# Kernel optimization log

Hardware: AMD Instinct MI355X
Metric: run time of the kernel (lower is better)

Reference implementation:

```python
import jax, jax.numpy as jnp
import numpy as np

B, N, D = 16, 1024, 320
L, H, K = 256, 256, 5
PAIR_IN = 2 * D + 6 + L  # 902


def setup_inputs() -> dict:
    key = jax.random.key(0)
    ks = jax.random.split(key, 8)
    return {
        "object_features": jax.random.normal(ks[0], (B, N, D), jnp.float32),
        "language_embedding": jax.random.normal(ks[1], (B, L), jnp.float32),
        "centers": jax.random.normal(ks[2], (B, N, 3), jnp.float32),
        "sizes": jax.random.uniform(ks[3], (B, N, 3), jnp.float32),
        "object_mask": jnp.ones((B, N), dtype=bool),
        "W1": jax.random.normal(ks[4], (PAIR_IN, H), jnp.float32) * 0.02,
        "b1": jnp.zeros((H,), jnp.float32),
        "W2": jax.random.normal(ks[5], (H, 1), jnp.float32) * 0.02,
        "b2": jnp.zeros((1,), jnp.float32),
    }


def _gather_neighbors(x, idx):
    # x: [B, N, C], idx: [B, N, k] -> [B, N, k, C]
    b, n, c = x.shape
    k = idx.shape[-1]
    flat = jnp.take_along_axis(x, idx.reshape(b, n * k)[..., None], axis=1)
    return flat.reshape(b, n, k, c)


def reference(object_features, language_embedding, centers, sizes, object_mask,
              W1, b1, W2, b2):
    b, n, d = object_features.shape
    k = min(K, n - 1)
    # pairwise squared distances [B, N, N]
    diff = centers[:, :, None, :] - centers[:, None, :, :]
    dist = jnp.sum(diff * diff, axis=-1)
    pair_mask = object_mask[:, :, None] & object_mask[:, None, :]
    dist = jnp.where(pair_mask, dist, jnp.inf)
    dist = jnp.where(jnp.eye(n, dtype=bool)[None], jnp.inf, dist)
    # k nearest neighbors (smallest distance)
    _, neighbor_indices = jax.lax.top_k(-dist, k)  # [B, N, k]

    neighbor_feats = _gather_neighbors(object_features, neighbor_indices)  # [B,N,k,D]
    neighbor_centers = _gather_neighbors(centers, neighbor_indices)        # [B,N,k,3]
    neighbor_sizes = _gather_neighbors(sizes, neighbor_indices)            # [B,N,k,3]

    rel_pos = (centers[:, :, None, :] - neighbor_centers) / 5.0
    rel_size = (sizes[:, :, None, :] - neighbor_sizes) / 2.0

    feat_i = jnp.broadcast_to(object_features[:, :, None, :], (b, n, k, d))
    lang = jnp.broadcast_to(language_embedding[:, None, None, :], (b, n, k, language_embedding.shape[-1]))
    pair_input = jnp.concatenate([feat_i, neighbor_feats, rel_pos, rel_size, lang], axis=-1)

    # relation MLP (dropout is identity in eval)
    h = jax.nn.relu(jnp.einsum('bnkp,ph->bnkh', pair_input, W1) + b1)
    scores = (jnp.einsum('bnkh,ho->bnko', h, W2) + b2)[..., 0]  # [B,N,k]
    weights = jax.nn.softmax(scores, axis=2)

    context = jnp.einsum('bnk,bnkd->bnd', weights, neighbor_feats)
    enhanced = object_features + context  # use_residual=True
    return enhanced, weights, neighbor_indices
```

## Files before the change

### kernel.cpp

```cpp
#include <hip/hip_runtime.h>
#include <math.h>

#define NB 16
#define NN 1024
#define ND 320
#define NL 256
#define NH 256
#define NK 5
#define KE 352

typedef short bf16x8 __attribute__((ext_vector_type(8)));
typedef float f32x4 __attribute__((ext_vector_type(4)));

__device__ inline ushort f2bf(float f) {
    unsigned u = __float_as_uint(f);
    u += 0x7fff + ((u >> 16) & 1);
    return (ushort)(u >> 16);
}
__device__ inline float bf2f(ushort u) {
    return __uint_as_float(((unsigned)u) << 16);
}

__global__ __launch_bounds__(256) void mini_prep_kernel(const float* __restrict__ W1,
                                                        ushort* __restrict__ W1T,
                                                        const float* __restrict__ lang,
                                                        const float* __restrict__ b1,
                                                        float* __restrict__ LP) {
    __shared__ float red[4][64];
    int bid = blockIdx.x;
    if (bid < 512) {
        int n = bid;
        int rowbase = (n < 256) ? 0 : 320;
        int col = n & 255;
        float sign = (n < 256) ? 1.f : -1.f;
        for (int k = threadIdx.x; k < KE; k += 256) {
            float v;
            if (k < 320) v = W1[(rowbase + k) * NH + col];
            else if (k < 326) v = sign * W1[(640 + (k - 320)) * NH + col];
            else v = 0.f;
            W1T[n * KE + k] = f2bf(v);
        }
        return;
    }
    int id = bid - 512;
    int b = id >> 2, hq = id & 3;
    int w = threadIdx.x >> 6, lane = threadIdx.x & 63;
    int h = hq * 64 + lane;
    const float* lb = lang + b * NL;
    float acc = 0.f;
    int l0 = w * 64;
#pragma unroll 8
    for (int l = 0; l < 64; ++l)
        acc = fmaf(lb[l0 + l], W1[(646 + l0 + l) * NH + h], acc);
    red[w][lane] = acc;
    __syncthreads();
    if (w == 0)
        LP[b * NH + h] = b1[h] + red[0][lane] + red[1][lane]
                       + red[2][lane] + red[3][lane];
}

#define LDP 40
__global__ __launch_bounds__(256) void mfma_gemm_kernel(const float* __restrict__ A32,
                                                        const float* __restrict__ C3,
                                                        const float* __restrict__ S3,
                                                        const ushort* __restrict__ BT,
                                                        ushort* __restrict__ P) {
    __shared__ ushort Als[128 * LDP];
    __shared__ ushort Bls[128 * LDP];
    int t = threadIdx.x;
    int lane = t & 63;
    int w = t >> 6;
    int wrow = (w >> 1) * 64, wcol = (w & 1) * 64;
    int m0 = blockIdx.x * 128, n0 = blockIdx.y * 128;
    int lr = lane & 15;
    int lg = lane >> 4;

    f32x4 zero = {0.f, 0.f, 0.f, 0.f};
    f32x4 acc[4][4];
#pragma unroll
    for (int i = 0; i < 4; ++i)
#pragma unroll
        for (int j = 0; j < 4; ++j) acc[i][j] = zero;

    for (int ks = 0; ks < 11; ++ks) {
        int k0 = ks * 32;
#pragma unroll
        for (int it = 0; it < 2; ++it) {
            int s = it * 256 + t;
            int r = s >> 2, q = s & 3;
            int4 pk;
            if (ks < 10) {
                const float* src = &A32[(m0 + r) * ND + k0 + q * 8];
                float4 v0 = *(const float4*)src;
                float4 v1 = *(const float4*)(src + 4);
                pk.x = (int)f2bf(v0.x) | ((int)f2bf(v0.y) << 16);
                pk.y = (int)f2bf(v0.z) | ((int)f2bf(v0.w) << 16);
                pk.z = (int)f2bf(v1.x) | ((int)f2bf(v1.y) << 16);
                pk.w = (int)f2bf(v1.z) | ((int)f2bf(v1.w) << 16);
            } else {
                pk.x = 0; pk.y = 0; pk.z = 0; pk.w = 0;
                if (q == 0) {
                    int m = m0 + r;
                    float c0 = C3[m * 3 + 0] * 0.2f;
                    float c1 = C3[m * 3 + 1] * 0.2f;
                    float c2 = C3[m * 3 + 2] * 0.2f;
                    float s0 = S3[m * 3 + 0] * 0.5f;
                    float s1 = S3[m * 3 + 1] * 0.5f;
                    float s2 = S3[m * 3 + 2] * 0.5f;
                    pk.x = (int)f2bf(c0) | ((int)f2bf(c1) << 16);
                    pk.y = (int)f2bf(c2) | ((int)f2bf(s0) << 16);
                    pk.z = (int)f2bf(s1) | ((int)f2bf(s2) << 16);
                }
            }
            *(int4*)&Als[r * LDP + q * 8] = pk;
            *(int4*)&Bls[r * LDP + q * 8] =
                *(const int4*)&BT[(n0 + r) * KE + k0 + q * 8];
        }
        __syncthreads();
        bf16x8 af[4], bfr[4];
#pragma unroll
        for (int i = 0; i < 4; ++i) {
            af[i]  = *(bf16x8*)&Als[(wrow + i * 16 + lr) * LDP + lg * 8];
            bfr[i] = *(bf16x8*)&Bls[(wcol + i * 16 + lr) * LDP + lg * 8];
        }
#pragma unroll
        for (int i = 0; i < 4; ++i)
#pragma unroll
            for (int j = 0; j < 4; ++j)
                acc[i][j] = __builtin_amdgcn_mfma_f32_16x16x32_bf16(af[i], bfr[j],
                                                                    acc[i][j], 0, 0, 0);
        __syncthreads();
    }

#pragma unroll
    for (int i = 0; i < 4; ++i) {
#pragma unroll
        for (int j = 0; j < 4; ++j) {
            int col = n0 + wcol + j * 16 + lr;
#pragma unroll
            for (int e = 0; e < 4; ++e) {
                int row = m0 + wrow + i * 16 + lg * 4 + e;
                P[row * 512 + col] = f2bf(acc[i][j][e]);
            }
        }
    }
}

#define INS(d, j, D0, D1, D2, D3, D4, I0, I1, I2, I3, I4)                      \
    {                                                                          \
        bool c0 = d < D0, c1 = d < D1, c2 = d < D2, c3 = d < D3, c4 = d < D4;  \
        D4 = c4 ? (c3 ? D3 : d) : D4;  I4 = c4 ? (c3 ? I3 : j) : I4;           \
        D3 = c3 ? (c2 ? D2 : d) : D3;  I3 = c3 ? (c2 ? I2 : j) : I3;           \
        D2 = c2 ? (c1 ? D1 : d) : D2;  I2 = c2 ? (c1 ? I1 : j) : I2;           \
        D1 = c1 ? (c0 ? D0 : d) : D1;  I1 = c1 ? (c0 ? I0 : j) : I1;           \
        D0 = c0 ? d : D0;              I0 = c0 ? j : I0;                       \
    }

__global__ __launch_bounds__(256) void knn_score_kernel(const float* __restrict__ feats,
                                                        const float* __restrict__ centers,
                                                        const ushort* __restrict__ P,
                                                        const float* __restrict__ LP,
                                                        const float* __restrict__ W2,
                                                        const float* __restrict__ b2,
                                                        float* __restrict__ enhanced,
                                                        float* __restrict__ weights,
                                                        float* __restrict__ idx_f) {
    __shared__ float cxs[NN], cys[NN], czs[NN];
    int wave = threadIdx.x >> 6;
    int lane = threadIdx.x & 63;
    int sbid = (blockIdx.x & 7) * 256 + (blockIdx.x >> 3);
    int wv = sbid * 4 + wave;
    int rowA = wv * 2, rowB = rowA | 1;
    int b = rowA >> 10;
    int iA = rowA & (NN - 1), iB = iA + 1;

    const float* cbase = centers + b * (NN * 3);
    for (int j = threadIdx.x; j < NN; j += 256) {
        int o = j * 3;
        cxs[j] = cbase[o]; cys[j] = cbase[o + 1]; czs[j] = cbase[o + 2];
    }
    __syncthreads();

    float pxA = cxs[iA], pyA = cys[iA], pzA = czs[iA];
    float pxB = cxs[iB], pyB = cys[iB], pzB = czs[iB];

    float dA0 = INFINITY, dA1 = INFINITY, dA2 = INFINITY, dA3 = INFINITY, dA4 = INFINITY;
    float dB0 = INFINITY, dB1 = INFINITY, dB2 = INFINITY, dB3 = INFINITY, dB4 = INFINITY;
    int iA0 = -1, iA1 = -1, iA2 = -1, iA3 = -1, iA4 = -1;
    int iB0 = -1, iB1 = -1, iB2 = -1, iB3 = -1, iB4 = -1;

#pragma unroll
    for (int tt = 0; tt < 16; ++tt) {
        int j = tt * 64 + lane;
        float cx = cxs[j], cy = cys[j], cz = czs[j];
        float dxA = pxA - cx, dyA = pyA - cy, dzA = pzA - cz;
        float dA = fmaf(dzA, dzA, fmaf(dyA, dyA, dxA * dxA));
        dA = (j == iA) ? INFINITY : dA;
        float dxB = pxB - cx, dyB = pyB - cy, dzB = pzB - cz;
        float dB = fmaf(dzB, dzB, fmaf(dyB, dyB, dxB * dxB));
        dB = (j == iB) ? INFINITY : dB;
        INS(dA, j, dA0, dA1, dA2, dA3, dA4, iA0, iA1, iA2, iA3, iA4);
        INS(dB, j, dB0, dB1, dB2, dB3, dB4, iB0, iB1, iB2, iB3, iB4);
    }

    int jnA[NK], jnB[NK];
#pragma unroll
    for (int k = 0; k < NK; ++k) {
        float mdA = dA0, mdB = dB0;
        int mjA = iA0, mjB = iB0;
#pragma unroll
        for (int off = 32; off > 0; off >>= 1) {
            float odA = __shfl_xor(mdA, off);
            int ojA = __shfl_xor(mjA, off);
            float odB = __shfl_xor(mdB, off);
            int ojB = __shfl_xor(mjB, off);
            bool tA = (odA < mdA) || ((odA == mdA) && ((unsigned)ojA < (unsigned)mjA));
            bool tB = (odB < mdB) || ((odB == mdB) && ((unsigned)ojB < (unsigned)mjB));
            mdA = tA ? odA : mdA;  mjA = tA ? ojA : mjA;
            mdB = tB ? odB : mdB;  mjB = tB ? ojB : mjB;
        }
        jnA[k] = mjA;
        jnB[k] = mjB;
        bool cA = (iA0 == mjA);
        dA0 = cA ? dA1 : dA0;  iA0 = cA ? iA1 : iA0;
        dA1 = cA ? dA2 : dA1;  iA1 = cA ? iA2 : iA1;
        dA2 = cA ? dA3 : dA2;  iA2 = cA ? iA3 : iA2;
        dA3 = cA ? dA4 : dA3;  iA3 = cA ? iA4 : iA3;
        dA4 = cA ? INFINITY : dA4;
        bool cB = (iB0 == mjB);
        dB0 = cB ? dB1 : dB0;  iB0 = cB ? iB1 : iB0;
        dB1 = cB ? dB2 : dB1;  iB1 = cB ? iB2 : iB1;
        dB2 = cB ? dB3 : dB2;  iB2 = cB ? iB3 : iB2;
        dB3 = cB ? dB4 : dB3;  iB3 = cB ? iB4 : iB3;
        dB4 = cB ? INFINITY : dB4;
    }

    if (lane == 0) {
#pragma unroll
        for (int k = 0; k < NK; ++k) {
            idx_f[rowA * NK + k] = (float)jnA[k];
            idx_f[rowB * NK + k] = (float)jnB[k];
        }
    }

    float4 lpv = ((const float4*)LP)[b * 64 + lane];
    ushort4 pfA = *(const ushort4*)&P[rowA * 512 + (lane << 2)];
    ushort4 pfB = *(const ushort4*)&P[rowB * 512 + (lane << 2)];
    float4 baseA = make_float4(bf2f(pfA.x) + lpv.x, bf2f(pfA.y) + lpv.y,
                               bf2f(pfA.z) + lpv.z, bf2f(pfA.w) + lpv.w);
    float4 baseB = make_float4(bf2f(pfB.x) + lpv.x, bf2f(pfB.y) + lpv.y,
                               bf2f(pfB.z) + lpv.z, bf2f(pfB.w) + lpv.w);
    float4 w2v = ((const float4*)W2)[lane];
    float b2v = b2[0];

    int pbase = (b << 10) * 512 + 256 + (lane << 2);
    float pA[NK], pB[NK];
#pragma unroll
    for (int k = 0; k < NK; ++k) {
        ushort4 pnA = *(const ushort4*)&P[pbase + jnA[k] * 512];
        ushort4 pnB = *(const ushort4*)&P[pbase + jnB[k] * 512];
        float hx = fmaxf(baseA.x + bf2f(pnA.x), 0.f);
        float hy = fmaxf(baseA.y + bf2f(pnA.y), 0.f);
        float hz = fmaxf(baseA.z + bf2f(pnA.z), 0.f);
        float hw = fmaxf(baseA.w + bf2f(pnA.w), 0.f);
        pA[k] = hx * w2v.x + hy * w2v.y + hz * w2v.z + hw * w2v.w;
        hx = fmaxf(baseB.x + bf2f(pnB.x), 0.f);
        hy = fmaxf(baseB.y + bf2f(pnB.y), 0.f);
        hz = fmaxf(baseB.z + bf2f(pnB.z), 0.f);
        hw = fmaxf(baseB.w + bf2f(pnB.w), 0.f);
        pB[k] = hx * w2v.x + hy * w2v.y + hz * w2v.z + hw * w2v.w;
    }

#pragma unroll
    for (int off = 32; off > 0; off >>= 1) {
        pA[0] += __shfl_xor(pA[0], off);
        pA[1] += __shfl_xor(pA[1], off);
        pA[2] += __shfl_xor(pA[2], off);
        pA[3] += __shfl_xor(pA[3], off);
        pA[4] += __shfl_xor(pA[4], off);
        pB[0] += __shfl_xor(pB[0], off);
        pB[1] += __shfl_xor(pB[1], off);
        pB[2] += __shfl_xor(pB[2], off);
        pB[3] += __shfl_xor(pB[3], off);
        pB[4] += __shfl_xor(pB[4], off);
    }

    float wkA[NK], wkB[NK];
    {
        float mxA = pA[0], mxB = pB[0];
#pragma unroll
        for (int k = 1; k < NK; ++k) { mxA = fmaxf(mxA, pA[k]); mxB = fmaxf(mxB, pB[k]); }
        float sA = 0.f, sB = 0.f;
#pragma unroll
        for (int k = 0; k < NK; ++k) {
            wkA[k] = __expf(pA[k] - mxA); sA += wkA[k];
            wkB[k] = __expf(pB[k] - mxB); sB += wkB[k];
        }
        float ivA = 1.f / sA, ivB = 1.f / sB;
#pragma unroll
        for (int k = 0; k < NK; ++k) { wkA[k] *= ivA; wkB[k] *= ivB; }
    }

    if (lane == 0) {
#pragma unroll
        for (int k = 0; k < NK; ++k) {
            weights[rowA * NK + k] = wkA[k];
            weights[rowB * NK + k] = wkB[k];
        }
    }

    const float* fb = feats + b * (NN * ND);
    {
        int dA_ = rowA * ND + (lane << 2);
        int dB_ = rowB * ND + (lane << 2);
        float4 aA = *(const float4*)&feats[dA_];
        float4 aB = *(const float4*)&feats[dB_];
#pragma unroll
        for (int k = 0; k < NK; ++k) {
            float4 nA = *(const float4*)&fb[jnA[k] * ND + (lane << 2)];
            float4 nB = *(const float4*)&fb[jnB[k] * ND + (lane << 2)];
            aA.x = fmaf(wkA[k], nA.x, aA.x); aA.y = fmaf(wkA[k], nA.y, aA.y);
            aA.z = fmaf(wkA[k], nA.z, aA.z); aA.w = fmaf(wkA[k], nA.w, aA.w);
            aB.x = fmaf(wkB[k], nB.x, aB.x); aB.y = fmaf(wkB[k], nB.y, aB.y);
            aB.z = fmaf(wkB[k], nB.z, aB.z); aB.w = fmaf(wkB[k], nB.w, aB.w);
        }
        *(float4*)&enhanced[dA_] = aA;
        *(float4*)&enhanced[dB_] = aB;
    }
    if (lane < 16) {
        int d0 = 256 + (lane << 2);
        float4 aA = *(const float4*)&feats[rowA * ND + d0];
        float4 aB = *(const float4*)&feats[rowB * ND + d0];
#pragma unroll
        for (int k = 0; k < NK; ++k) {
            float4 nA = *(const float4*)&fb[jnA[k] * ND + d0];
            float4 nB = *(const float4*)&fb[jnB[k] * ND + d0];
            aA.x = fmaf(wkA[k], nA.x, aA.x); aA.y = fmaf(wkA[k], nA.y, aA.y);
            aA.z = fmaf(wkA[k], nA.z, aA.z); aA.w = fmaf(wkA[k], nA.w, aA.w);
            aB.x = fmaf(wkB[k], nB.x, aB.x); aB.y = fmaf(wkB[k], nB.y, aB.y);
            aB.z = fmaf(wkB[k], nB.z, aB.z); aB.w = fmaf(wkB[k], nB.w, aB.w);
        }
        *(float4*)&enhanced[rowA * ND + d0] = aA;
        *(float4*)&enhanced[rowB * ND + d0] = aB;
    }
}

extern "C" void kernel_launch(void* const* d_in, const int* in_sizes, int n_in,
                              void* d_out, int out_size, void* d_ws, size_t ws_size,
                              hipStream_t stream) {
    const float* feats   = (const float*)d_in[0];
    const float* lang    = (const float*)d_in[1];
    const float* centers = (const float*)d_in[2];
    const float* sizes   = (const float*)d_in[3];
    const float* W1 = (const float*)d_in[5];
    const float* b1 = (const float*)d_in[6];
    const float* W2 = (const float*)d_in[7];
    const float* b2 = (const float*)d_in[8];

    float* out = (float*)d_out;
    float* enhanced = out;
    float* weights  = out + (size_t)NB * NN * ND;
    float* idx_f    = weights + (size_t)NB * NN * NK;

    char* ws = (char*)d_ws;
    ushort* P   = (ushort*)ws;
    ushort* W1T = (ushort*)(ws + 16777216);
    float*  LP  = (float*)(ws + 16777216 + 360448);

    mini_prep_kernel<<<dim3(576), 256, 0, stream>>>(W1, W1T, lang, b1, LP);
    mfma_gemm_kernel<<<dim3(128, 4), 256, 0, stream>>>(feats, centers, sizes, W1T, P);
    knn_score_kernel<<<dim3(2048), 256, 0, stream>>>(feats, centers, P, LP,
                                                     W2, b2,
                                                     enhanced, weights, idx_f);
}
```

Measured before the change: 62.85 us.

## Prefetch GEMM tiles into registers and remap blocks to XCDs

The GEMM main loop now loads the next K-slice of features and weights into registers while the current slice's MFMAs run, so global load latency overlaps compute. The final centers/sizes slice is peeled out of the loop. The grid becomes 1-D with an XCD-aware block-to-tile mapping, so blocks that share A rows land on the same chiplet's L2. This raises register pressure and lengthens the code, and the remapping assumes round-robin dispatch across 8 XCDs. The unused b2 load in the score kernel is also dropped.

```diff
diff --git a/kernel.cpp b/kernel.cpp
--- a/kernel.cpp
+++ b/kernel.cpp
@@ -67,14 +67,20 @@
                                                         ushort* __restrict__ P) {
     __shared__ ushort Als[128 * LDP];
     __shared__ ushort Bls[128 * LDP];
+    int bid = blockIdx.x;
+    int xcd = bid & 7;
+    int local = bid >> 3;
+    int m0 = (xcd * 16 + (local >> 2)) * 128;
+    int n0 = (local & 3) * 128;
     int t = threadIdx.x;
     int lane = t & 63;
     int w = t >> 6;
     int wrow = (w >> 1) * 64, wcol = (w & 1) * 64;
-    int m0 = blockIdx.x * 128, n0 = blockIdx.y * 128;
     int lr = lane & 15;
     int lg = lane >> 4;
 
+    int rr = t >> 2, q = t & 3;
+
     f32x4 zero = {0.f, 0.f, 0.f, 0.f};
     f32x4 acc[4][4];
 #pragma unroll
@@ -82,41 +88,56 @@
 #pragma unroll
         for (int j = 0; j < 4; ++j) acc[i][j] = zero;
 
-    for (int ks = 0; ks < 11; ++ks) {
-        int k0 = ks * 32;
+    float4 v0[2], v1[2];
+    int4 pb[2];
+#pragma unroll
+    for (int it = 0; it < 2; ++it) {
+        int r = rr + it * 64;
+        const float* src = &A32[(m0 + r) * ND + q * 8];
+        v0[it] = *(const float4*)src;
+        v1[it] = *(const float4*)(src + 4);
+        pb[it] = *(const int4*)&BT[(n0 + r) * KE + q * 8];
+    }
+    float cs0 = 0.f, cs1 = 0.f, cs2 = 0.f, cs3 = 0.f, cs4 = 0.f, cs5 = 0.f;
+    float cs6 = 0.f, cs7 = 0.f, cs8 = 0.f, cs9 = 0.f, cs10 = 0.f, cs11 = 0.f;
+
+    for (int ks = 0; ks < 10; ++ks) {
 #pragma unroll
         for (int it = 0; it < 2; ++it) {
-            int s = it * 256 + t;
-            int r = s >> 2, q = s & 3;
+            int r = rr + it * 64;
             int4 pk;
-            if (ks < 10) {
+            pk.x = (int)f2bf(v0[it].x) | ((int)f2bf(v0[it].y) << 16);
+            pk.y = (int)f2bf(v0[it].z) | ((int)f2bf(v0[it].w) << 16);
+            pk.z = (int)f2bf(v1[it].x) | ((int)f2bf(v1[it].y) << 16);
+            pk.w = (int)f2bf(v1[it].z) | ((int)f2bf(v1[it].w) << 16);
+            *(int4*)&Als[r * LDP + q * 8] = pk;
+            *(int4*)&Bls[r * LDP + q * 8] = pb[it];
+        }
+        __syncthreads();
+        if (ks < 9) {
+            int k0 = (ks + 1) * 32;
+#pragma unroll
+            for (int it = 0; it < 2; ++it) {
+                int r = rr + it * 64;
                 const float* src = &A32[(m0 + r) * ND + k0 + q * 8];
-                float4 v0 = *(const float4*)src;
-                float4 v1 = *(const float4*)(src + 4);
-                pk.x = (int)f2bf(v0.x) | ((int)f2bf(v0.y) << 16);
-                pk.y = (int)f2bf(v0.z) | ((int)f2bf(v0.w) << 16);
-                pk.z = (int)f2bf(v1.x) | ((int)f2bf(v1.y) << 16);
-                pk.w = (int)f2bf(v1.z) | ((int)f2bf(v1.w) << 16);
-            } else {
-                pk.x = 0; pk.y = 0; pk.z = 0; pk.w = 0;
-                if (q == 0) {
-                    int m = m0 + r;
-                    float c0 = C3[m * 3 + 0] * 0.2f;
-                    float c1 = C3[m * 3 + 1] * 0.2f;
-                    float c2 = C3[m * 3 + 2] * 0.2f;
-                    float s0 = S3[m * 3 + 0] * 0.5f;
-                    float s1 = S3[m * 3 + 1] * 0.5f;
-                    float s2 = S3[m * 3 + 2] * 0.5f;
-                    pk.x = (int)f2bf(c0) | ((int)f2bf(c1) << 16);
-                    pk.y = (int)f2bf(c2) | ((int)f2bf(s0) << 16);
-                    pk.z = (int)f2bf(s1) | ((int)f2bf(s2) << 16);
-                }
+                v0[it] = *(const float4*)src;
+                v1[it] = *(const float4*)(src + 4);
+                pb[it] = *(const int4*)&BT[(n0 + r) * KE + k0 + q * 8];
             }
-            *(int4*)&Als[r * LDP + q * 8] = pk;
-            *(int4*)&Bls[r * LDP + q * 8] =
-                *(const int4*)&BT[(n0 + r) * KE + k0 + q * 8];
-        }
-        __syncthreads();
+        } else {
+            if (q == 0) {
+                int mA = m0 + rr, mB = m0 + rr + 64;
+                cs0 = C3[mA * 3 + 0]; cs1 = C3[mA * 3 + 1]; cs2 = C3[mA * 3 + 2];
+                cs3 = S3[mA * 3 + 0]; cs4 = S3[mA * 3 + 1]; cs5 = S3[mA * 3 + 2];
+                cs6 = C3[mB * 3 + 0]; cs7 = C3[mB * 3 + 1]; cs8 = C3[mB * 3 + 2];
+                cs9 = S3[mB * 3 + 0]; cs10 = S3[mB * 3 + 1]; cs11 = S3[mB * 3 + 2];
+            }
+#pragma unroll
+            for (int it = 0; it < 2; ++it) {
+                int r = rr + it * 64;
+                pb[it] = *(const int4*)&BT[(n0 + r) * KE + 320 + q * 8];
+            }
+        }
         bf16x8 af[4], bfr[4];
 #pragma unroll
         for (int i = 0; i < 4; ++i) {
@@ -130,6 +151,37 @@
                 acc[i][j] = __builtin_amdgcn_mfma_f32_16x16x32_bf16(af[i], bfr[j],
                                                                     acc[i][j], 0, 0, 0);
         __syncthreads();
+    }
+
+    {
+        int4 pkA;
+        pkA.x = (int)f2bf(cs0 * 0.2f) | ((int)f2bf(cs1 * 0.2f) << 16);
+        pkA.y = (int)f2bf(cs2 * 0.2f) | ((int)f2bf(cs3 * 0.5f) << 16);
+        pkA.z = (int)f2bf(cs4 * 0.5f) | ((int)f2bf(cs5 * 0.5f) << 16);
+        pkA.w = 0;
+        int4 pkB;
+        pkB.x = (int)f2bf(cs6 * 0.2f) | ((int)f2bf(cs7 * 0.2f) << 16);
+        pkB.y = (int)f2bf(cs8 * 0.2f) | ((int)f2bf(cs9 * 0.5f) << 16);
+        pkB.z = (int)f2bf(cs10 * 0.5f) | ((int)f2bf(cs11 * 0.5f) << 16);
+        pkB.w = 0;
+        int4 zq = {0, 0, 0, 0};
+        *(int4*)&Als[rr * LDP + q * 8] = (q == 0) ? pkA : zq;
+        *(int4*)&Als[(rr + 64) * LDP + q * 8] = (q == 0) ? pkB : zq;
+        *(int4*)&Bls[rr * LDP + q * 8] = pb[0];
+        *(int4*)&Bls[(rr + 64) * LDP + q * 8] = pb[1];
+        __syncthreads();
+        bf16x8 af[4], bfr[4];
+#pragma unroll
+        for (int i = 0; i < 4; ++i) {
+            af[i]  = *(bf16x8*)&Als[(wrow + i * 16 + lr) * LDP + lg * 8];
+            bfr[i] = *(bf16x8*)&Bls[(wcol + i * 16 + lr) * LDP + lg * 8];
+        }
+#pragma unroll
+        for (int i = 0; i < 4; ++i)
+#pragma unroll
+            for (int j = 0; j < 4; ++j)
+                acc[i][j] = __builtin_amdgcn_mfma_f32_16x16x32_bf16(af[i], bfr[j],
+                                                                    acc[i][j], 0, 0, 0);
     }
 
 #pragma unroll
@@ -251,7 +303,6 @@
     float4 baseB = make_float4(bf2f(pfB.x) + lpv.x, bf2f(pfB.y) + lpv.y,
                                bf2f(pfB.z) + lpv.z, bf2f(pfB.w) + lpv.w);
     float4 w2v = ((const float4*)W2)[lane];
-    float b2v = b2[0];
 
     int pbase = (b << 10) * 512 + 256 + (lane << 2);
     float pA[NK], pB[NK];
@@ -368,7 +419,7 @@
     float*  LP  = (float*)(ws + 16777216 + 360448);
 
     mini_prep_kernel<<<dim3(576), 256, 0, stream>>>(W1, W1T, lang, b1, LP);
-    mfma_gemm_kernel<<<dim3(128, 4), 256, 0, stream>>>(feats, centers, sizes, W1T, P);
+    mfma_gemm_kernel<<<dim3(512), 256, 0, stream>>>(feats, centers, sizes, W1T, P);
     knn_score_kernel<<<dim3(2048), 256, 0, stream>>>(feats, centers, P, LP,
                                                      W2, b2,
                                                      enhanced, weights, idx_f);
```

After: 69.32 us. 1.1x slower.
